# Kernel optimization log

Measured on AMD Instinct MI355X. Metric: run time of the kernel, lower is better.

Reference implementation:

```python
import jax, jax.numpy as jnp
import numpy as np

B, T, D, H, TW = 4, 2048, 2048, 8, 4
DH = D // H


def setup_inputs() -> dict:
    key = jax.random.key(0)
    ks = jax.random.split(key, 16)
    s = lambda k, shape, std: jax.random.normal(k, shape, dtype=jnp.float32) * std
    inp = {
        "x": jax.random.normal(ks[0], (B, T, D), dtype=jnp.float32),
        "segment_pos": jnp.tile(jnp.arange(T, dtype=jnp.int32), (B, 1)),
        # linear_y / linear_x: width -> lru_width, std = 1/sqrt(width)
        "Wy": s(ks[1], (D, D), (1.0 / D) ** 0.5),
        "by": jnp.zeros((D,), jnp.float32),
        "Wx": s(ks[2], (D, D), (1.0 / D) ** 0.5),
        "bx": jnp.zeros((D,), jnp.float32),
        # depthwise causal conv: [temporal_width, lru_width]
        "conv_w": s(ks[3], (TW, D), (1.0 / TW) ** 0.5),
        "conv_b": jnp.zeros((D,), jnp.float32),
        # RG-LRU block-diagonal gates: [H, D/H, D/H]
        "gx_w": s(ks[4], (H, DH, DH), (1.0 / DH) ** 0.5),
        "gx_b": jnp.zeros((H, DH), jnp.float32),
        "ga_w": s(ks[5], (H, DH, DH), (1.0 / DH) ** 0.5),
        "ga_b": jnp.zeros((H, DH), jnp.float32),
        # a_param: softplus(a_param) > 0 controls decay rate
        "a_param": jnp.log(jnp.exp(jax.random.uniform(ks[6], (D,), minval=0.3, maxval=0.9)) - 1.0 + 1e-6),
        # linear_out: lru_width -> width, std = 1/sqrt(lru_width)
        "Wout": s(ks[7], (D, D), (1.0 / D) ** 0.5),
        "bout": jnp.zeros((D,), jnp.float32),
    }
    return inp


def _causal_conv1d(x, w, b, segment_pos):
    # depthwise causal conv over time; contributions from other segments masked
    t = x.shape[1]
    acc = jnp.zeros_like(x)
    for i in range(TW):
        shift = TW - 1 - i  # input at t - shift, weighted by w[i]
        xs = x if shift == 0 else jnp.pad(x, ((0, 0), (shift, 0), (0, 0)))[:, :t]
        mask = (segment_pos >= shift)[..., None].astype(x.dtype)
        acc = acc + xs * mask * w[i]
    return acc + b


def _rg_lru(x, segment_pos, gx_w, gx_b, ga_w, ga_b, a_param):
    b, t, d = x.shape
    xr = x.reshape(b, t, H, DH)
    gate_x = jax.nn.sigmoid(jnp.einsum("bthi,hij->bthj", xr, gx_w) + gx_b).reshape(b, t, d)
    gate_a = jax.nn.sigmoid(jnp.einsum("bthi,hij->bthj", xr, ga_w) + ga_b).reshape(b, t, d)
    log_a = -8.0 * gate_a * jax.nn.softplus(a_param)  # [B,T,D]
    a = jnp.exp(log_a)
    reset = (segment_pos == 0)[..., None]  # [B,T,1]
    multiplier = jnp.sqrt(jnp.maximum(1.0 - jnp.exp(2.0 * log_a), 0.0))
    multiplier = jnp.where(reset, 1.0, multiplier)
    normed = x * gate_x * multiplier
    a_scan = jnp.where(reset, 0.0, a)

    def step(h, inputs):
        a_t, x_t = inputs
        h = a_t * h + x_t
        return h, h

    h0 = jnp.zeros((b, d), x.dtype)
    _, ys = jax.lax.scan(step, h0, (a_scan.transpose(1, 0, 2), normed.transpose(1, 0, 2)))
    return ys.transpose(1, 0, 2)


def reference(x, segment_pos, Wy, by, Wx, bx, conv_w, conv_b, gx_w, gx_b, ga_w, ga_b, a_param, Wout, bout):
    y = jax.nn.gelu(x @ Wy.T + by, approximate=True)
    x_proj = x @ Wx.T + bx
    x_conv = _causal_conv1d(x_proj, conv_w, conv_b, segment_pos)
    x_lru = _rg_lru(x_conv, segment_pos, gx_w, gx_b, ga_w, ga_b, a_param)
    out = (x_lru * y) @ Wout.T + bout
    return out
```

## Files before the change

kernel.cpp:

```cpp
#include <hip/hip_runtime.h>
#include <cstdint>
#include <cstddef>

typedef __bf16 bf16;
typedef __bf16 bf16x8 __attribute__((ext_vector_type(8)));
typedef float f32x4 __attribute__((ext_vector_type(4)));

#define BDIM 4
#define TDIM 2048
#define DDIM 2048
#define HDIM 8
#define DHD 256
#define MTOT 8192
#define NCHUNK 64
#define LCHUNK 32

__device__ __forceinline__ void stage16(const bf16* g, bf16* l) {
  __builtin_amdgcn_global_load_lds(
      (const __attribute__((address_space(1))) void*)g,
      (__attribute__((address_space(3))) void*)l, 16, 0, 0);
}

#define BARX() __builtin_amdgcn_s_barrier()
#define SCHB() __builtin_amdgcn_sched_barrier(0)
#define WAITVM(N) asm volatile("s_waitcnt vmcnt(" #N ")")
#define WAITLG(N) asm volatile("s_waitcnt lgkmcnt(" #N ")")

__device__ __forceinline__ float sigmoid_f(float x) {
  return __fdividef(1.f, 1.f + __expf(-x));
}
__device__ __forceinline__ float gelu_tanh(float v) {
  float u = 0.7978845608028654f * (v + 0.044715f * v * v * v);
  u = fminf(fmaxf(u, -15.f), 15.f);
  float t = __expf(2.f * u);
  return 0.5f * v * (1.f + __fdividef(t - 1.f, t + 1.f));
}
__device__ __forceinline__ float softplus_f(float x) {
  return __logf(1.f + __expf(x));
}

__global__ __launch_bounds__(256) void f2b(const float* __restrict__ src,
                                           bf16* __restrict__ dst) {
  size_t i = ((size_t)blockIdx.x * 256 + threadIdx.x) * 8;
  const float4 a = *(const float4*)(src + i);
  const float4 b = *(const float4*)(src + i + 4);
  bf16x8 r;
  r[0] = (bf16)a.x; r[1] = (bf16)a.y; r[2] = (bf16)a.z; r[3] = (bf16)a.w;
  r[4] = (bf16)b.x; r[5] = (bf16)b.y; r[6] = (bf16)b.z; r[7] = (bf16)b.w;
  *(bf16x8*)(dst + i) = r;
}

template <typename TO, int EPI>
__global__ __launch_bounds__(512, 2) void gemm256(
    const bf16* __restrict__ A, const bf16* __restrict__ Bm,
    const float* __restrict__ bias, TO* __restrict__ C,
    int K, int lda, int ldb, int ldc) {
  const int gx = gridDim.x, gy = gridDim.y;
  const int nwg = gx * gy;
  const int did = blockIdx.x + gx * blockIdx.y;
  const int cpx = nwg >> 3;
  const int lid = (did & 7) * cpx + (did >> 3);
  const int n0 = (lid % gx) * 256;
  const int m0 = (lid / gx) * 256;

  __shared__ bf16 sA0[256 * 64];
  __shared__ bf16 sA1[256 * 64];
  __shared__ bf16 sB0[256 * 64];
  __shared__ bf16 sB1[256 * 64];
  const int tid = threadIdx.x;
  const int lane = tid & 63;
  const int wid = tid >> 6;
  const int wr = wid >> 2;
  const int wc = wid & 3;
  const int quad = lane >> 4;
  const int l15 = lane & 15;

  const int sr = tid >> 3;
  const int ks8 = ((tid & 7) ^ (sr & 7)) << 3;
  const bf16* Ag = A + (size_t)(m0 + sr) * lda + ks8;
  const bf16* Bg = Bm + (size_t)(n0 + sr) * ldb + ks8;

  const int swz0 = ((quad) ^ (l15 & 7)) << 3;
  const int swz1 = ((4 + quad) ^ (l15 & 7)) << 3;

  f32x4 acc[8][4];
#pragma unroll
  for (int i = 0; i < 8; ++i)
#pragma unroll
    for (int j = 0; j < 4; ++j)
#pragma unroll
      for (int r = 0; r < 4; ++r) acc[i][j][r] = 0.f;

  const int NT = K >> 6;

#define STG_A(ARR, H, TK)                                                     \
  do {                                                                        \
    _Pragma("unroll") for (int j_ = 0; j_ < 2; ++j_) {                        \
      const int c_ = (H) * 2 + j_;                                            \
      stage16(Ag + (size_t)(c_ * 64) * lda + (size_t)(TK) * 64,               \
              &ARR[(c_ * 64 + wid * 8) * 64]);                                \
    }                                                                         \
  } while (0)
#define STG_B(ARR, H, TK)                                                     \
  do {                                                                        \
    _Pragma("unroll") for (int j_ = 0; j_ < 2; ++j_) {                        \
      const int c_ = (H) * 2 + j_;                                            \
      stage16(Bg + (size_t)(c_ * 64) * ldb + (size_t)(TK) * 64,               \
              &ARR[(c_ * 64 + wid * 8) * 64]);                                \
    }                                                                         \
  } while (0)

  bf16x8 af[4][2], b0[2][2], b1[2][2];

#define RDA(MH, ARR)                                                          \
  do {                                                                        \
    _Pragma("unroll") for (int mi_ = 0; mi_ < 4; ++mi_) {                     \
      const int arow_ = wr * 128 + (MH) * 64 + mi_ * 16 + l15;                \
      af[mi_][0] = *(const bf16x8*)(&ARR[arow_ * 64] + swz0);                 \
      af[mi_][1] = *(const bf16x8*)(&ARR[arow_ * 64] + swz1);                 \
    }                                                                         \
  } while (0)
#define RDB(DST, NH, ARR)                                                     \
  do {                                                                        \
    _Pragma("unroll") for (int ni_ = 0; ni_ < 2; ++ni_) {                     \
      const int brow_ = wc * 64 + (NH) * 32 + ni_ * 16 + l15;                 \
      DST[ni_][0] = *(const bf16x8*)(&ARR[brow_ * 64] + swz0);                \
      DST[ni_][1] = *(const bf16x8*)(&ARR[brow_ * 64] + swz1);                \
    }                                                                         \
  } while (0)
#define MFMAQ(MH, NH, BB)                                                     \
  do {                                                                        \
    __builtin_amdgcn_s_setprio(1);                                            \
    _Pragma("unroll") for (int mi_ = 0; mi_ < 4; ++mi_)                       \
        _Pragma("unroll") for (int ni_ = 0; ni_ < 2; ++ni_) {                 \
      acc[(MH)*4 + mi_][(NH)*2 + ni_] = __builtin_amdgcn_mfma_f32_16x16x32_bf16( \
          af[mi_][0], BB[ni_][0], acc[(MH)*4 + mi_][(NH)*2 + ni_], 0, 0, 0);  \
      acc[(MH)*4 + mi_][(NH)*2 + ni_] = __builtin_amdgcn_mfma_f32_16x16x32_bf16( \
          af[mi_][1], BB[ni_][1], acc[(MH)*4 + mi_][(NH)*2 + ni_], 0, 0, 0);  \
    }                                                                         \
    __builtin_amdgcn_s_setprio(0);                                            \
  } while (0)

#define TILE(SAs, SBs, SAo, SBo, T)                                           \
  do {                                                                        \
    const int tn_ = ((T) + 1 < NT) ? (T) + 1 : NT - 1;                        \
    const int tnn_ = ((T) + 2 < NT) ? (T) + 2 : NT - 1;                       \
                                                           \
    RDA(0, SAs);                                                              \
    RDB(b0, 0, SBs);                                                          \
    STG_A(SAo, 1, tn_);                                                       \
    WAITLG(8);                                                                \
    BARX();                                                                   \
    WAITLG(0);                                                                \
    SCHB();                                                                   \
    MFMAQ(0, 0, b0);                                                          \
    BARX();                                                                   \
                                                            \
    RDB(b1, 1, SBs);                                                          \
    STG_B(SBo, 1, tn_);                                                       \
    BARX();                                                                   \
    WAITLG(0);                                                                \
    SCHB();                                                                   \
    MFMAQ(0, 1, b1);                                                          \
    BARX();                                                                   \
                                                 \
    RDA(1, SAs);                                                              \
    STG_B(SBs, 0, tnn_);                                                      \
    BARX();                                                                   \
    WAITLG(0);                                                                \
    SCHB();                                                                   \
    MFMAQ(1, 0, b0);                                                          \
    BARX();                                                                   \
                                  \
    STG_A(SAs, 0, tnn_);                                                      \
    BARX();                                                                   \
    SCHB();                                                                   \
    MFMAQ(1, 1, b1);                                                          \
    WAITVM(4);                                                                \
    BARX();                                                                   \
  } while (0)

  STG_B(sB0, 0, 0); STG_A(sA0, 0, 0);
  STG_A(sA0, 1, 0); STG_B(sB0, 1, 0);
  STG_B(sB1, 0, 1); STG_A(sA1, 0, 1);
  WAITVM(4);
  SCHB();
  BARX();

  for (int t = 0; t < NT; t += 2) {
    TILE(sA0, sB0, sA1, sB1, t);
    TILE(sA1, sB1, sA0, sB0, t + 1);
  }
  WAITVM(0);

#undef STG_A
#undef STG_B
#undef RDA
#undef RDB
#undef MFMAQ
#undef TILE

  float bv[4];
#pragma unroll
  for (int nn = 0; nn < 4; ++nn) bv[nn] = bias[n0 + wc * 64 + nn * 16 + l15];
#pragma unroll
  for (int mm = 0; mm < 8; ++mm) {
#pragma unroll
    for (int r = 0; r < 4; ++r) {
      const int m = m0 + wr * 128 + mm * 16 + quad * 4 + r;
      TO* Crow = C + (size_t)m * ldc + n0 + wc * 64 + l15;
#pragma unroll
      for (int nn = 0; nn < 4; ++nn) {
        float v = acc[mm][nn][r] + bv[nn];
        if (EPI == 1) v = gelu_tanh(v);
        Crow[nn * 16] = (TO)v;
      }
    }
  }
}

__global__ __launch_bounds__(256) void gate_gemm(
    const bf16* __restrict__ xconv,
    const bf16* __restrict__ gxT, const bf16* __restrict__ gaT,
    bf16* __restrict__ gxr, bf16* __restrict__ gar) {
  const int h = blockIdx.z >> 1;
  const int g = blockIdx.z & 1;
  const bf16* A = xconv + h * DHD;
  const bf16* Bm = (g ? gaT : gxT) + (size_t)h * DHD * DHD;
  bf16* C = (g ? gar : gxr) + h * DHD;
  const int n0 = blockIdx.x * 128;
  const int m0 = blockIdx.y * 128;
  __shared__ bf16 As[128 * 32];
  __shared__ bf16 Bs[128 * 32];
  const int tid = threadIdx.x;
  const int lane = tid & 63;
  const int wid = tid >> 6;
  const int waveM = wid >> 1, waveN = wid & 1;
  const int quad = lane >> 4;
  const int l15 = lane & 15;
  const int srow = lane >> 2;
  const int scol = (lane & 3) * 8;

  f32x4 acc[4][4];
#pragma unroll
  for (int i = 0; i < 4; ++i)
#pragma unroll
    for (int j = 0; j < 4; ++j)
#pragma unroll
      for (int r = 0; r < 4; ++r) acc[i][j][r] = 0.f;

  for (int k0 = 0; k0 < DHD; k0 += 32) {
    if (k0) __syncthreads();
#pragma unroll
    for (int cc = 0; cc < 2; ++cc) {
      const int q = wid * 2 + cc;
      const int row = q * 16 + srow;
      stage16(A + (size_t)(m0 + row) * DDIM + k0 + scol, As + q * 512);
      stage16(Bm + (size_t)(n0 + row) * DHD + k0 + scol, Bs + q * 512);
    }
    __syncthreads();
    bf16x8 af[4], bfr[4];
#pragma unroll
    for (int i = 0; i < 4; ++i) {
      af[i]  = *(const bf16x8*)&As[(waveM * 64 + i * 16 + l15) * 32 + quad * 8];
      bfr[i] = *(const bf16x8*)&Bs[(waveN * 64 + i * 16 + l15) * 32 + quad * 8];
    }
#pragma unroll
    for (int i = 0; i < 4; ++i)
#pragma unroll
      for (int j = 0; j < 4; ++j)
        acc[i][j] = __builtin_amdgcn_mfma_f32_16x16x32_bf16(af[i], bfr[j], acc[i][j], 0, 0, 0);
  }

#pragma unroll
  for (int j = 0; j < 4; ++j) {
    const int n = n0 + waveN * 64 + j * 16 + l15;
#pragma unroll
    for (int i = 0; i < 4; ++i) {
#pragma unroll
      for (int r = 0; r < 4; ++r) {
        const int m = m0 + waveM * 64 + i * 16 + quad * 4 + r;
        C[(size_t)m * DDIM + n] = (bf16)acc[i][j][r];
      }
    }
  }
}

__global__ __launch_bounds__(256) void conv_kernel(
    const bf16* __restrict__ xp, const float* __restrict__ cw,
    const float* __restrict__ cb, const int* __restrict__ segp,
    bf16* __restrict__ xc) {
  int v = blockIdx.x * 256 + threadIdx.x;
  int dv = v & (DDIM / 8 - 1);
  int m = v >> 8;
  int d0 = dv * 8;
  int t = m & (TDIM - 1);
  int sp = segp[m];
  float acc[8];
#pragma unroll
  for (int j = 0; j < 8; ++j) acc[j] = cb[d0 + j];
#pragma unroll
  for (int i = 0; i < 4; ++i) {
    int shift = 3 - i;
    if (t >= shift && sp >= shift) {
      bf16x8 xv = *(const bf16x8*)&xp[(size_t)(m - shift) * DDIM + d0];
#pragma unroll
      for (int j = 0; j < 8; ++j) acc[j] = fmaf((float)xv[j], cw[i * DDIM + d0 + j], acc[j]);
    }
  }
  bf16x8 o;
#pragma unroll
  for (int j = 0; j < 8; ++j) o[j] = (bf16)acc[j];
  *(bf16x8*)&xc[(size_t)m * DDIM + d0] = o;
}

__global__ __launch_bounds__(256) void transpose_gates(
    const float* __restrict__ gxw, const float* __restrict__ gaw,
    bf16* __restrict__ gxT, bf16* __restrict__ gaT) {
  __shared__ bf16 tile[32][33];
  int zz = blockIdx.z;
  int h = zz >> 1;
  const float* src = (zz & 1) ? gaw : gxw;
  bf16* dst = (zz & 1) ? gaT : gxT;
  int j0 = blockIdx.x * 32;
  int i0 = blockIdx.y * 32;
  int r = threadIdx.x >> 5;
  int c = threadIdx.x & 31;
  for (int rr = r; rr < 32; rr += 8)
    tile[rr][c] = (bf16)src[(size_t)(h * DHD + i0 + rr) * DHD + j0 + c];
  __syncthreads();
  for (int rr = r; rr < 32; rr += 8)
    dst[(size_t)(h * DHD + j0 + rr) * DHD + i0 + c] = tile[c][rr];
}

__device__ __forceinline__ void lru_elem(float pgx, float pga, float xc,
                                         float spv, bool reset,
                                         float& a, float& nr) {
  const float gx = sigmoid_f(pgx);
  const float ga = sigmoid_f(pga);
  const float la = -8.f * ga * spv;
  a = reset ? 0.f : __expf(la);
  const float mult = reset ? 1.f : sqrtf(fmaxf(1.f - __expf(2.f * la), 0.f));
  nr = xc * gx * mult;
}

__global__ __launch_bounds__(256) void scan_phase1(
    const bf16* __restrict__ gxr, const bf16* __restrict__ gar,
    const bf16* __restrict__ xconv,
    const float* __restrict__ gxb, const float* __restrict__ gab,
    const float* __restrict__ apar, const int* __restrict__ segp,
    float* __restrict__ chA, float* __restrict__ chH) {
  int idx = blockIdx.x * 256 + threadIdx.x;
  int d = idx & (DDIM - 1);
  int c = (idx >> 11) & (NCHUNK - 1);
  int b = idx >> 17;
  const float gxbv = gxb[d], gabv = gab[d];
  const float spv = softplus_f(apar[d]);
  const int mrow = b * TDIM + c * LCHUNK;
  size_t base = (size_t)mrow * DDIM + d;
  float A = 1.f, hh = 0.f;
  for (int i = 0; i < LCHUNK; ++i) {
    size_t o = base + (size_t)i * DDIM;
    float a, nr;
    lru_elem((float)gxr[o] + gxbv, (float)gar[o] + gabv, (float)xconv[o],
             spv, segp[mrow + i] == 0, a, nr);
    hh = fmaf(a, hh, nr);
    A *= a;
  }
  int ci = (b * NCHUNK + c) * DDIM + d;
  chA[ci] = A;
  chH[ci] = hh;
}

__global__ __launch_bounds__(256) void scan_phase2(
    const float* __restrict__ chA, const float* __restrict__ chH,
    float* __restrict__ hst) {
  int idx = blockIdx.x * 256 + threadIdx.x;
  int d = idx & (DDIM - 1);
  int b = idx >> 11;
  float s = 0.f;
  for (int c = 0; c < NCHUNK; ++c) {
    int ci = (b * NCHUNK + c) * DDIM + d;
    hst[ci] = s;
    s = fmaf(chA[ci], s, chH[ci]);
  }
}

__global__ __launch_bounds__(256) void scan_phase3(
    const bf16* __restrict__ gxr, const bf16* __restrict__ gar,
    const bf16* __restrict__ xconv,
    const float* __restrict__ gxb, const float* __restrict__ gab,
    const float* __restrict__ apar, const int* __restrict__ segp,
    const float* __restrict__ hst, bf16* __restrict__ yz) {
  int idx = blockIdx.x * 256 + threadIdx.x;
  int d = idx & (DDIM - 1);
  int c = (idx >> 11) & (NCHUNK - 1);
  int b = idx >> 17;
  const float gxbv = gxb[d], gabv = gab[d];
  const float spv = softplus_f(apar[d]);
  const int mrow = b * TDIM + c * LCHUNK;
  size_t base = (size_t)mrow * DDIM + d;
  float hh = hst[(b * NCHUNK + c) * DDIM + d];
  for (int i = 0; i < LCHUNK; ++i) {
    size_t o = base + (size_t)i * DDIM;
    float a, nr;
    lru_elem((float)gxr[o] + gxbv, (float)gar[o] + gabv, (float)xconv[o],
             spv, segp[mrow + i] == 0, a, nr);
    hh = fmaf(a, hh, nr);
    yz[o] = (bf16)(hh * (float)yz[o]);
  }
}

extern "C" void kernel_launch(void* const* d_in, const int* in_sizes, int n_in,
                              void* d_out, int out_size, void* d_ws, size_t ws_size,
                              hipStream_t stream) {
  const float* x    = (const float*)d_in[0];
  const int*   segp = (const int*)d_in[1];
  const float* Wy   = (const float*)d_in[2];
  const float* by   = (const float*)d_in[3];
  const float* Wx   = (const float*)d_in[4];
  const float* bx   = (const float*)d_in[5];
  const float* cw   = (const float*)d_in[6];
  const float* cb   = (const float*)d_in[7];
  const float* gxw  = (const float*)d_in[8];
  const float* gxb  = (const float*)d_in[9];
  const float* gaw  = (const float*)d_in[10];
  const float* gab  = (const float*)d_in[11];
  const float* apar = (const float*)d_in[12];
  const float* Wout = (const float*)d_in[13];
  const float* bout = (const float*)d_in[14];

  const size_t MD = (size_t)MTOT * DDIM;
  const size_t WD = (size_t)DDIM * DDIM;
  bf16* xb    = (bf16*)d_out;
  bf16* xproj = (bf16*)((char*)d_out + MD * 2);
  bf16* xconv = xb;
  bf16* gxr   = xproj;

  char* ws = (char*)d_ws;
  bf16*  gar = (bf16*)ws;
  bf16*  W1  = (bf16*)(ws + MD * 2);
  bf16*  WB1 = (bf16*)(ws + 2 * MD * 2);
  bf16*  WB2 = (bf16*)(ws + 2 * MD * 2 + WD * 2);
  char*  tail = ws + 2 * MD * 2 + 2 * WD * 2;
  const size_t GW = (size_t)HDIM * DHD * DHD * 2;
  const size_t CH = (size_t)BDIM * NCHUNK * DDIM * 4;
  bf16*  gxT = (bf16*)tail;
  bf16*  gaT = (bf16*)(tail + GW);
  float* chA = (float*)(tail + 2 * GW);
  float* chH = (float*)(tail + 2 * GW + CH);
  float* hst = (float*)(tail + 2 * GW + 2 * CH);

  dim3 blk(256);
  f2b<<<dim3(MD / 2048), blk, 0, stream>>>(x, xb);
  f2b<<<dim3(WD / 2048), blk, 0, stream>>>(Wx, WB1);
  f2b<<<dim3(WD / 2048), blk, 0, stream>>>(Wy, WB2);
  transpose_gates<<<dim3(8, 8, 16), blk, 0, stream>>>(gxw, gaw, gxT, gaT);

  gemm256<bf16, 0><<<dim3(8, 32), dim3(512), 0, stream>>>(xb, WB1, bx, xproj, DDIM, DDIM, DDIM, DDIM);
  gemm256<bf16, 1><<<dim3(8, 32), dim3(512), 0, stream>>>(xb, WB2, by, W1, DDIM, DDIM, DDIM, DDIM);

  conv_kernel<<<dim3(MTOT * (DDIM / 8) / 256), blk, 0, stream>>>(xproj, cw, cb, segp, xconv);

  gate_gemm<<<dim3(2, 64, 16), blk, 0, stream>>>(xconv, gxT, gaT, gxr, gar);

  scan_phase1<<<dim3(BDIM * NCHUNK * DDIM / 256), blk, 0, stream>>>(
      gxr, gar, xconv, gxb, gab, apar, segp, chA, chH);
  scan_phase2<<<dim3(BDIM * DDIM / 256), blk, 0, stream>>>(chA, chH, hst);
  scan_phase3<<<dim3(BDIM * NCHUNK * DDIM / 256), blk, 0, stream>>>(
      gxr, gar, xconv, gxb, gab, apar, segp, hst, W1);

  f2b<<<dim3(WD / 2048), blk, 0, stream>>>(Wout, WB1);
  gemm256<float, 0><<<dim3(8, 32), dim3(512), 0, stream>>>(W1, WB1, bout, (float*)d_out, DDIM, DDIM, DDIM, DDIM);
}
```

Before: 435.3 us.

## Replace 256x256 GEMM with 128x128 tile kernel and merge input projections

Replaces the 512-thread 256x256-tile GEMM with a 256-thread 128x128-tile kernel that has a simpler two-phase pipeline and fewer barriers and LDS waits. The two input projections (Wx and Wy) now run in a single launch, with blockIdx.z choosing the weight, bias, output and GELU epilogue. The aim is more workgroups for better CU occupancy and load balance, less synchronisation, and one fewer launch. In exchange, the smaller tiles lower operand reuse per block and raise global/L2 traffic, and removing the explicit lgkmcnt waits makes the kernel depend on compiler-inserted waits.

```diff
diff --git a/kernel.cpp b/kernel.cpp
--- a/kernel.cpp
+++ b/kernel.cpp
@@ -24,7 +24,6 @@
 #define BARX() __builtin_amdgcn_s_barrier()
 #define SCHB() __builtin_amdgcn_sched_barrier(0)
 #define WAITVM(N) asm volatile("s_waitcnt vmcnt(" #N ")")
-#define WAITLG(N) asm volatile("s_waitcnt lgkmcnt(" #N ")")
 
 __device__ __forceinline__ float sigmoid_f(float x) {
   return __fdividef(1.f, 1.f + __expf(-x));
@@ -50,28 +49,35 @@
   *(bf16x8*)(dst + i) = r;
 }
 
-template <typename TO, int EPI>
-__global__ __launch_bounds__(512, 2) void gemm256(
-    const bf16* __restrict__ A, const bf16* __restrict__ Bm,
-    const float* __restrict__ bias, TO* __restrict__ C,
+template <typename TO>
+__global__ __launch_bounds__(256, 2) void gemm128(
+    const bf16* __restrict__ A,
+    const bf16* __restrict__ B0m, const bf16* __restrict__ B1m,
+    const float* __restrict__ bias0, const float* __restrict__ bias1,
+    TO* __restrict__ C0, TO* __restrict__ C1, int epi1,
     int K, int lda, int ldb, int ldc) {
+  const bf16* Bm = blockIdx.z ? B1m : B0m;
+  const float* bias = blockIdx.z ? bias1 : bias0;
+  TO* C = blockIdx.z ? C1 : C0;
+  const int EPI = blockIdx.z ? epi1 : 0;
+
   const int gx = gridDim.x, gy = gridDim.y;
   const int nwg = gx * gy;
   const int did = blockIdx.x + gx * blockIdx.y;
   const int cpx = nwg >> 3;
   const int lid = (did & 7) * cpx + (did >> 3);
-  const int n0 = (lid % gx) * 256;
-  const int m0 = (lid / gx) * 256;
-
-  __shared__ bf16 sA0[256 * 64];
-  __shared__ bf16 sA1[256 * 64];
-  __shared__ bf16 sB0[256 * 64];
-  __shared__ bf16 sB1[256 * 64];
+  const int n0 = (lid % gx) * 128;
+  const int m0 = (lid / gx) * 128;
+
+  __shared__ bf16 sA0[128 * 64];
+  __shared__ bf16 sA1[128 * 64];
+  __shared__ bf16 sB0[128 * 64];
+  __shared__ bf16 sB1[128 * 64];
   const int tid = threadIdx.x;
   const int lane = tid & 63;
   const int wid = tid >> 6;
-  const int wr = wid >> 2;
-  const int wc = wid & 3;
+  const int wr = wid >> 1;
+  const int wc = wid & 1;
   const int quad = lane >> 4;
   const int l15 = lane & 15;
 
@@ -83,9 +89,9 @@
   const int swz0 = ((quad) ^ (l15 & 7)) << 3;
   const int swz1 = ((4 + quad) ^ (l15 & 7)) << 3;
 
-  f32x4 acc[8][4];
-#pragma unroll
-  for (int i = 0; i < 8; ++i)
+  f32x4 acc[4][4];
+#pragma unroll
+  for (int i = 0; i < 4; ++i)
 #pragma unroll
     for (int j = 0; j < 4; ++j)
 #pragma unroll
@@ -93,29 +99,25 @@
 
   const int NT = K >> 6;
 
-#define STG_A(ARR, H, TK)                                                     \
-  do {                                                                        \
-    _Pragma("unroll") for (int j_ = 0; j_ < 2; ++j_) {                        \
-      const int c_ = (H) * 2 + j_;                                            \
-      stage16(Ag + (size_t)(c_ * 64) * lda + (size_t)(TK) * 64,               \
-              &ARR[(c_ * 64 + wid * 8) * 64]);                                \
-    }                                                                         \
-  } while (0)
-#define STG_B(ARR, H, TK)                                                     \
-  do {                                                                        \
-    _Pragma("unroll") for (int j_ = 0; j_ < 2; ++j_) {                        \
-      const int c_ = (H) * 2 + j_;                                            \
-      stage16(Bg + (size_t)(c_ * 64) * ldb + (size_t)(TK) * 64,               \
-              &ARR[(c_ * 64 + wid * 8) * 64]);                                \
-    }                                                                         \
+#define STG_A(ARR, TK)                                                        \
+  do {                                                                        \
+    _Pragma("unroll") for (int c_ = 0; c_ < 4; ++c_)                          \
+        stage16(Ag + (size_t)(c_ * 32) * lda + (size_t)(TK) * 64,             \
+                &ARR[(c_ * 32 + wid * 8) * 64]);                              \
+  } while (0)
+#define STG_B(ARR, TK)                                                        \
+  do {                                                                        \
+    _Pragma("unroll") for (int c_ = 0; c_ < 4; ++c_)                          \
+        stage16(Bg + (size_t)(c_ * 32) * ldb + (size_t)(TK) * 64,             \
+                &ARR[(c_ * 32 + wid * 8) * 64]);                              \
   } while (0)
 
   bf16x8 af[4][2], b0[2][2], b1[2][2];
 
-#define RDA(MH, ARR)                                                          \
+#define RDA(ARR)                                                              \
   do {                                                                        \
     _Pragma("unroll") for (int mi_ = 0; mi_ < 4; ++mi_) {                     \
-      const int arow_ = wr * 128 + (MH) * 64 + mi_ * 16 + l15;                \
+      const int arow_ = wr * 64 + mi_ * 16 + l15;                             \
       af[mi_][0] = *(const bf16x8*)(&ARR[arow_ * 64] + swz0);                 \
       af[mi_][1] = *(const bf16x8*)(&ARR[arow_ * 64] + swz1);                 \
     }                                                                         \
@@ -128,15 +130,15 @@
       DST[ni_][1] = *(const bf16x8*)(&ARR[brow_ * 64] + swz1);                \
     }                                                                         \
   } while (0)
-#define MFMAQ(MH, NH, BB)                                                     \
+#define MFMAQ(NH, BB)                                                         \
   do {                                                                        \
     __builtin_amdgcn_s_setprio(1);                                            \
     _Pragma("unroll") for (int mi_ = 0; mi_ < 4; ++mi_)                       \
         _Pragma("unroll") for (int ni_ = 0; ni_ < 2; ++ni_) {                 \
-      acc[(MH)*4 + mi_][(NH)*2 + ni_] = __builtin_amdgcn_mfma_f32_16x16x32_bf16( \
-          af[mi_][0], BB[ni_][0], acc[(MH)*4 + mi_][(NH)*2 + ni_], 0, 0, 0);  \
-      acc[(MH)*4 + mi_][(NH)*2 + ni_] = __builtin_amdgcn_mfma_f32_16x16x32_bf16( \
-          af[mi_][1], BB[ni_][1], acc[(MH)*4 + mi_][(NH)*2 + ni_], 0, 0, 0);  \
+      acc[mi_][(NH)*2 + ni_] = __builtin_amdgcn_mfma_f32_16x16x32_bf16(       \
+          af[mi_][0], BB[ni_][0], acc[mi_][(NH)*2 + ni_], 0, 0, 0);           \
+      acc[mi_][(NH)*2 + ni_] = __builtin_amdgcn_mfma_f32_16x16x32_bf16(       \
+          af[mi_][1], BB[ni_][1], acc[mi_][(NH)*2 + ni_], 0, 0, 0);           \
     }                                                                         \
     __builtin_amdgcn_s_setprio(0);                                            \
   } while (0)
@@ -145,44 +147,23 @@
   do {                                                                        \
     const int tn_ = ((T) + 1 < NT) ? (T) + 1 : NT - 1;                        \
     const int tnn_ = ((T) + 2 < NT) ? (T) + 2 : NT - 1;                       \
-                                                           \
-    RDA(0, SAs);                                                              \
+                                                                     \
+    RDA(SAs);                                                                 \
     RDB(b0, 0, SBs);                                                          \
-    STG_A(SAo, 1, tn_);                                                       \
-    WAITLG(8);                                                                \
+    STG_B(SBo, tn_);                                                          \
+    MFMAQ(0, b0);                                                             \
     BARX();                                                                   \
-    WAITLG(0);                                                                \
-    SCHB();                                                                   \
-    MFMAQ(0, 0, b0);                                                          \
-    BARX();                                                                   \
-                                                            \
+                                                                     \
     RDB(b1, 1, SBs);                                                          \
-    STG_B(SBo, 1, tn_);                                                       \
-    BARX();                                                                   \
-    WAITLG(0);                                                                \
-    SCHB();                                                                   \
-    MFMAQ(0, 1, b1);                                                          \
-    BARX();                                                                   \
-                                                 \
-    RDA(1, SAs);                                                              \
-    STG_B(SBs, 0, tnn_);                                                      \
-    BARX();                                                                   \
-    WAITLG(0);                                                                \
-    SCHB();                                                                   \
-    MFMAQ(1, 0, b0);                                                          \
-    BARX();                                                                   \
-                                  \
-    STG_A(SAs, 0, tnn_);                                                      \
-    BARX();                                                                   \
-    SCHB();                                                                   \
-    MFMAQ(1, 1, b1);                                                          \
+    STG_A(SAs, tnn_);                                                         \
+    MFMAQ(1, b1);                                                             \
     WAITVM(4);                                                                \
     BARX();                                                                   \
   } while (0)
 
-  STG_B(sB0, 0, 0); STG_A(sA0, 0, 0);
-  STG_A(sA0, 1, 0); STG_B(sB0, 1, 0);
-  STG_B(sB1, 0, 1); STG_A(sA1, 0, 1);
+  const int t1 = (NT > 1) ? 1 : 0;
+  STG_B(sB0, 0); STG_A(sA0, 0);
+  STG_B(sB1, t1); STG_A(sA1, t1);
   WAITVM(4);
   SCHB();
   BARX();
@@ -204,10 +185,10 @@
 #pragma unroll
   for (int nn = 0; nn < 4; ++nn) bv[nn] = bias[n0 + wc * 64 + nn * 16 + l15];
 #pragma unroll
-  for (int mm = 0; mm < 8; ++mm) {
+  for (int mm = 0; mm < 4; ++mm) {
 #pragma unroll
     for (int r = 0; r < 4; ++r) {
-      const int m = m0 + wr * 128 + mm * 16 + quad * 4 + r;
+      const int m = m0 + wr * 64 + mm * 16 + quad * 4 + r;
       TO* Crow = C + (size_t)m * ldc + n0 + wc * 64 + l15;
 #pragma unroll
       for (int nn = 0; nn < 4; ++nn) {
@@ -457,8 +438,8 @@
   f2b<<<dim3(WD / 2048), blk, 0, stream>>>(Wy, WB2);
   transpose_gates<<<dim3(8, 8, 16), blk, 0, stream>>>(gxw, gaw, gxT, gaT);
 
-  gemm256<bf16, 0><<<dim3(8, 32), dim3(512), 0, stream>>>(xb, WB1, bx, xproj, DDIM, DDIM, DDIM, DDIM);
-  gemm256<bf16, 1><<<dim3(8, 32), dim3(512), 0, stream>>>(xb, WB2, by, W1, DDIM, DDIM, DDIM, DDIM);
+  gemm128<bf16><<<dim3(16, 64, 2), blk, 0, stream>>>(
+      xb, WB1, WB2, bx, by, xproj, W1, 1, DDIM, DDIM, DDIM, DDIM);
 
   conv_kernel<<<dim3(MTOT * (DDIM / 8) / 256), blk, 0, stream>>>(xproj, cw, cb, segp, xconv);
 
@@ -471,5 +452,7 @@
       gxr, gar, xconv, gxb, gab, apar, segp, hst, W1);
 
   f2b<<<dim3(WD / 2048), blk, 0, stream>>>(Wout, WB1);
-  gemm256<float, 0><<<dim3(8, 32), dim3(512), 0, stream>>>(W1, WB1, bout, (float*)d_out, DDIM, DDIM, DDIM, DDIM);
-}
+  gemm128<float><<<dim3(16, 64, 1), blk, 0, stream>>>(
+      W1, WB1, WB1, bout, bout, (float*)d_out, (float*)d_out, 0,
+      DDIM, DDIM, DDIM, DDIM);
+}
```

New measurement: 436.0 us. Within noise of the previous version (+0.2%).
